# Optimization experiments

Hardware: AMD Instinct MI355X
Metric: run time of the kernel (lower is better)

## Reference

```python
import jax, jax.numpy as jnp
import numpy as np

B, OUT, IN = 2048, 4096, 4096
KEEPRATE = 0.5  # mid-training drop schedule state; first-call default masks nothing


def setup_inputs() -> dict:
    key = jax.random.key(0)
    k1, k2, k3, k4 = jax.random.split(key, 4)
    data = jax.random.normal(k1, (B, IN), dtype=jnp.float32)
    # weight parameter = fftn of a real N(0, 0.1) matrix, stored as complex
    w0 = jax.random.normal(k2, (OUT, IN), dtype=jnp.float32) * 0.1
    wc = jnp.fft.fftn(w0.astype(jnp.float32))
    w_real = jnp.real(wc).astype(jnp.float32)
    w_imag = jnp.imag(wc).astype(jnp.float32)
    bias = jax.random.normal(k3, (OUT,), dtype=jnp.float32) * 0.1
    # ZMAT: rank assignment, a permutation of 0..OUT*IN-1
    zmat = jax.random.permutation(k4, jnp.arange(OUT * IN, dtype=jnp.int64)).reshape(OUT, IN)
    return {"data": data, "w_real": w_real, "w_imag": w_imag, "bias": bias, "zmat": zmat}


def reference(data, w_real, w_imag, bias, zmat):
    O, I = w_real.shape
    numel = O * I
    threval = KEEPRATE * numel
    # IDROP: keep entries whose rank <= threshold (ZMAT > threval -> 0)
    idrop = (zmat.astype(jnp.float32) <= threval).astype(w_real.dtype)
    dropweight = (w_real + 1j * w_imag) * idrop  # masked FFT-domain weight
    # torch.fft.irfftn(dropweight, s=(O, I)): full ifft on dim 0, real irfft on dim 1
    # (numpy/jax irfft crops the last axis to I//2+1, same as torch)
    w_spatial = jnp.fft.irfftn(dropweight, s=(O, I), axes=(0, 1)).astype(data.dtype)
    return data @ w_spatial.T + bias
```

## Files before the change

kernel.cpp:

```cpp
#include <hip/hip_runtime.h>
#include <hip/hip_bf16.h>
#include <stdint.h>

#define OUT_N 4096
#define IN_N  4096
#define BATCH 2048
#define KHALF 2049

typedef __bf16 bf16x8 __attribute__((ext_vector_type(8)));
typedef float  f32x4  __attribute__((ext_vector_type(4)));

__device__ __forceinline__ unsigned short f2bf(float f) {
  unsigned int u = __builtin_bit_cast(unsigned int, f);
  u += 0x7FFFu + ((u >> 16) & 1u);
  return (unsigned short)(u >> 16);
}

__device__ __forceinline__ float2 cmul(float2 a, float2 b) {
  return make_float2(a.x * b.x - a.y * b.y, a.x * b.y + a.y * b.x);
}
__device__ __forceinline__ float2 cadd(float2 a, float2 b) { return make_float2(a.x + b.x, a.y + b.y); }
__device__ __forceinline__ float2 csub(float2 a, float2 b) { return make_float2(a.x - b.x, a.y - b.y); }
__device__ __forceinline__ float2 muli(float2 a) { return make_float2(-a.y, a.x); }

__device__ __forceinline__ void dft4i(float2& x0, float2& x1, float2& x2, float2& x3) {
  float2 t0 = cadd(x0, x2), t1 = csub(x0, x2);
  float2 t2 = cadd(x1, x3), t3 = csub(x1, x3);
  float2 it3 = muli(t3);
  x0 = cadd(t0, t2); x2 = csub(t0, t2);
  x1 = cadd(t1, it3); x3 = csub(t1, it3);
}

#define C8f  0.70710678118654752f
#define C16f 0.92387953251128676f
#define S16f 0.38268343236508977f

__device__ __forceinline__ void dft16i(float2 r[16]) {
  float2 t[16];
#pragma unroll
  for (int b = 0; b < 4; ++b) {
    float2 a0 = r[b], a1 = r[4 + b], a2 = r[8 + b], a3 = r[12 + b];
    dft4i(a0, a1, a2, a3);
    t[b * 4 + 0] = a0; t[b * 4 + 1] = a1; t[b * 4 + 2] = a2; t[b * 4 + 3] = a3;
  }
  const float2 W1 = make_float2(C16f, S16f);
  const float2 W2 = make_float2(C8f, C8f);
  const float2 W3 = make_float2(S16f, C16f);
  const float2 W6 = make_float2(-C8f, C8f);
  const float2 W9 = make_float2(-C16f, -S16f);
  t[5]  = cmul(t[5],  W1);  t[6]  = cmul(t[6],  W2);  t[7]  = cmul(t[7],  W3);
  t[9]  = cmul(t[9],  W2);  t[10] = muli(t[10]);      t[11] = cmul(t[11], W6);
  t[13] = cmul(t[13], W3);  t[14] = cmul(t[14], W6);  t[15] = cmul(t[15], W9);
#pragma unroll
  for (int q = 0; q < 4; ++q) {
    float2 a0 = t[q], a1 = t[4 + q], a2 = t[8 + q], a3 = t[12 + q];
    dft4i(a0, a1, a2, a3);
    r[q] = a0; r[q + 4] = a1; r[q + 8] = a2; r[q + 12] = a3;
  }
}

__device__ __forceinline__ void twiddle16(float2 r[16], float theta) {
  float sn, cs;
  __sincosf(theta, &sn, &cs);
  float2 w = make_float2(cs, sn);
  float2 wk = w;
  r[1] = cmul(r[1], wk);
#pragma unroll
  for (int k = 2; k < 16; ++k) {
    wk = cmul(wk, w);
    r[k] = cmul(r[k], wk);
  }
}

__device__ void fft4096_core(float2 r[16], float2* lds, int t) {
  dft16i(r);
  twiddle16(r, 1.53398078788564123e-3f * (float)t);
#pragma unroll
  for (int k1 = 0; k1 < 16; ++k1) lds[k1 * 257 + t] = r[k1];
  __syncthreads();
  const int k1 = t & 15, b = t >> 4;
  float2 s[16];
#pragma unroll
  for (int a = 0; a < 16; ++a) s[a] = lds[k1 * 257 + 16 * a + b];
  __syncthreads();
  dft16i(s);
  twiddle16(s, 2.45436926061702596e-2f * (float)b);
#pragma unroll
  for (int c = 0; c < 16; ++c) lds[k1 * 273 + c * 17 + b] = s[c];
  __syncthreads();
#pragma unroll
  for (int bb = 0; bb < 16; ++bb) r[bb] = lds[k1 * 273 + b * 17 + bb];
  dft16i(r);
}

__global__ void mask_transpose(const float* __restrict__ wr, const float* __restrict__ wi,
                               const int* __restrict__ zmat, float2* __restrict__ wt) {
  __shared__ float2 tile[32][33];
  const int k0 = blockIdx.x * 32;
  const int o0 = blockIdx.y * 32;
  const int tx = threadIdx.x;
  const int ty = threadIdx.y;
#pragma unroll
  for (int r = 0; r < 4; ++r) {
    int o = o0 + ty + r * 8;
    int k = k0 + tx;
    float2 v = make_float2(0.f, 0.f);
    if (k < KHALF) {
      size_t idx = (size_t)o * IN_N + k;
      if (zmat[idx] <= 8388608) v = make_float2(wr[idx], wi[idx]);
    }
    tile[ty + r * 8][tx] = v;
  }
  __syncthreads();
#pragma unroll
  for (int r = 0; r < 4; ++r) {
    int k = k0 + ty + r * 8;
    int o = o0 + tx;
    if (k < KHALF) wt[(size_t)k * OUT_N + o] = tile[tx][ty + r * 8];
  }
}

__global__ __launch_bounds__(256) void col_ifft(float2* __restrict__ wt) {
  __shared__ float2 lds[4368];
  const int t = threadIdx.x;
  float2* row = wt + (size_t)blockIdx.x * OUT_N;
  float2 r[16];
#pragma unroll
  for (int n1 = 0; n1 < 16; ++n1) r[n1] = row[n1 * 256 + t];
  fft4096_core(r, lds, t);
#pragma unroll
  for (int d = 0; d < 16; ++d) row[t + 256 * d] = r[d];
}

__global__ void transpose_ko(const float2* __restrict__ yt, float2* __restrict__ y) {
  __shared__ float2 tile[32][33];
  const int k0 = blockIdx.x * 32;
  const int o0 = blockIdx.y * 32;
  const int tx = threadIdx.x;
  const int ty = threadIdx.y;
#pragma unroll
  for (int r = 0; r < 4; ++r) {
    int k = k0 + ty + r * 8;
    int o = o0 + tx;
    if (k < KHALF) tile[ty + r * 8][tx] = yt[(size_t)k * OUT_N + o];
  }
  __syncthreads();
#pragma unroll
  for (int r = 0; r < 4; ++r) {
    int o = o0 + ty + r * 8;
    int k = k0 + tx;
    if (k < KHALF) y[(size_t)o * KHALF + k] = tile[tx][ty + r * 8];
  }
}

__global__ __launch_bounds__(256) void row_irfft2(const float2* __restrict__ y,
                                                  unsigned short* __restrict__ wbf) {
  __shared__ float2 lds[4368];
  const int t = threadIdx.x;
  const int oa = blockIdx.x * 2, ob = oa + 1;
  const float2* rowa = y + (size_t)oa * KHALF;
  const float2* rowb = y + (size_t)ob * KHALF;
  float2* lsa = lds;
  float2* lsb = lds + 2049;
#pragma unroll
  for (int j = 0; j < 9; ++j) {
    int k = t + j * 256;
    if (k < KHALF) { lsa[k] = rowa[k]; lsb[k] = rowb[k]; }
  }
  __syncthreads();
  float2 r[16];
#pragma unroll
  for (int n1 = 0; n1 < 16; ++n1) {
    int m = n1 * 256 + t;
    float2 za, zb;
    if (m == 0)        { za = make_float2(lsa[0].x, 0.f);    zb = make_float2(lsb[0].x, 0.f); }
    else if (m < 2048) { za = lsa[m];                        zb = lsb[m]; }
    else if (m == 2048){ za = make_float2(lsa[2048].x, 0.f); zb = make_float2(lsb[2048].x, 0.f); }
    else { float2 ua = lsa[4096 - m], ub = lsb[4096 - m];
           za = make_float2(ua.x, -ua.y); zb = make_float2(ub.x, -ub.y); }
    r[n1] = make_float2(za.x - zb.y, za.y + zb.x);
  }
  __syncthreads();
  fft4096_core(r, lds, t);
  const float sc = 1.0f / (4096.0f * 4096.0f);
  unsigned short* orow_a = wbf + (size_t)oa * IN_N;
  unsigned short* orow_b = wbf + (size_t)ob * IN_N;
#pragma unroll
  for (int d = 0; d < 16; ++d) {
    orow_a[t + 256 * d] = f2bf(r[d].x * sc);
    orow_b[t + 256 * d] = f2bf(r[d].y * sc);
  }
}

__global__ void cvt_bf16(const float* __restrict__ x, unsigned short* __restrict__ o, int n4) {
  int i = blockIdx.x * blockDim.x + threadIdx.x;
  if (i < n4) {
    float4 v = ((const float4*)x)[i];
    ushort4 r;
    r.x = f2bf(v.x); r.y = f2bf(v.y); r.z = f2bf(v.z); r.w = f2bf(v.w);
    ((ushort4*)o)[i] = r;
  }
}

__device__ __forceinline__ void gload_lds16(const void* gp, void* lp) {
  typedef const __attribute__((address_space(1))) void* gptr_t;
  typedef __attribute__((address_space(3))) void* lptr_t;
  __builtin_amdgcn_global_load_lds((gptr_t)(unsigned long long)gp,
                                   (lptr_t)(unsigned int)(unsigned long long)lp,
                                   16, 0, 0);
}

__global__ __launch_bounds__(512) void gemm_bt_bias(const unsigned short* __restrict__ A,
                                                    const unsigned short* __restrict__ B,
                                                    const float* __restrict__ bias,
                                                    float* __restrict__ C) {
  __shared__ __align__(16) unsigned short As[128 * 32];
  __shared__ __align__(16) unsigned short Bs[128 * 32];
  const int tid  = threadIdx.x;
  const int wave = tid >> 6;
  const int lane = tid & 63;
  const int gm0 = blockIdx.y * 128;
  const int gn0 = blockIdx.x * 128;

  f32x4 acc[4][2] = {};
  const int wm = wave >> 2, wn = wave & 3;
  const int lrow = lane >> 2;
  const int lcol = (lane & 3) * 8;
  const int rbase = wave * 16;

  for (int kt = 0; kt < IN_N; kt += 32) {
    gload_lds16(A + ((size_t)(gm0 + rbase + lrow) * IN_N + kt + lcol),
                As + (size_t)rbase * 32);
    gload_lds16(B + ((size_t)(gn0 + rbase + lrow) * IN_N + kt + lcol),
                Bs + (size_t)rbase * 32);
    __syncthreads();

    bf16x8 af[4], bfr[2];
#pragma unroll
    for (int i = 0; i < 4; ++i)
      af[i]  = *(const bf16x8*)&As[(wm * 64 + i * 16 + (lane & 15)) * 32 + (lane >> 4) * 8];
#pragma unroll
    for (int j = 0; j < 2; ++j)
      bfr[j] = *(const bf16x8*)&Bs[(wn * 32 + j * 16 + (lane & 15)) * 32 + (lane >> 4) * 8];
#pragma unroll
    for (int mi = 0; mi < 4; ++mi)
#pragma unroll
      for (int ni = 0; ni < 2; ++ni)
        acc[mi][ni] = __builtin_amdgcn_mfma_f32_16x16x32_bf16(af[mi], bfr[ni], acc[mi][ni], 0, 0, 0);
    __syncthreads();
  }

  const int col0 = gn0 + wn * 32 + (lane & 15);
  const int row0 = gm0 + wm * 64 + (lane >> 4) * 4;
#pragma unroll
  for (int mi = 0; mi < 4; ++mi) {
#pragma unroll
    for (int ni = 0; ni < 2; ++ni) {
      int col = col0 + ni * 16;
      float bv = bias[col];
#pragma unroll
      for (int r = 0; r < 4; ++r) {
        int row = row0 + mi * 16 + r;
        C[(size_t)row * OUT_N + col] = acc[mi][ni][r] + bv;
      }
    }
  }
}

extern "C" void kernel_launch(void* const* d_in, const int* in_sizes, int n_in,
                              void* d_out, int out_size, void* d_ws, size_t ws_size,
                              hipStream_t stream) {
  const float* data = (const float*)d_in[0];
  const float* wr   = (const float*)d_in[1];
  const float* wi   = (const float*)d_in[2];
  const float* bias = (const float*)d_in[3];
  const int*   zmat = (const int*)d_in[4];

  char* ws = (char*)d_ws;
  float2* wt = (float2*)ws;
  float2* y  = (float2*)(ws + 67141632ull);
  unsigned short* wbf = (unsigned short*)ws;
  unsigned short* dbf = (unsigned short*)(ws + 33554432ull);

  hipLaunchKernelGGL(mask_transpose, dim3(65, 128), dim3(32, 8), 0, stream, wr, wi, zmat, wt);
  hipLaunchKernelGGL(col_ifft,       dim3(2049),    dim3(256),   0, stream, wt);
  hipLaunchKernelGGL(transpose_ko,   dim3(65, 128), dim3(32, 8), 0, stream, wt, y);
  hipLaunchKernelGGL(row_irfft2,     dim3(2048),    dim3(256),   0, stream, y, wbf);
  hipLaunchKernelGGL(cvt_bf16,       dim3(8192),    dim3(256),   0, stream, data, dbf, (BATCH * IN_N) / 4);
  hipLaunchKernelGGL(gemm_bt_bias,   dim3(OUT_N / 128, BATCH / 128), dim3(512), 0, stream,
                     dbf, wbf, bias, (float*)d_out);
}
```

Measured before the change: 377.3 us.

## Enlarge GEMM per-wave tile with BK=64 swizzled LDS and widen mask_transpose tiles

The GEMM now runs 4 waves per block instead of 8. Each wave computes a 64x64 output tile instead of 64x32, and each step loads a K-slice of 64. LDS chunks are XOR-swizzled to avoid bank conflicts, which raises register reuse and halves the number of barriers per K. Separately, mask_transpose processes 64 columns per block with vectorized float2/int2 loads, plus a dedicated block for the Nyquist column. The larger accumulator set raises register pressure and may lower occupancy.

```diff
diff --git a/kernel.cpp b/kernel.cpp
--- a/kernel.cpp
+++ b/kernel.cpp
@@ -95,28 +95,38 @@
 
 __global__ void mask_transpose(const float* __restrict__ wr, const float* __restrict__ wi,
                                const int* __restrict__ zmat, float2* __restrict__ wt) {
-  __shared__ float2 tile[32][33];
-  const int k0 = blockIdx.x * 32;
-  const int o0 = blockIdx.y * 32;
+  __shared__ float2 tile[32][65];
   const int tx = threadIdx.x;
   const int ty = threadIdx.y;
+  const int o0 = blockIdx.y * 32;
+  if (blockIdx.x == 32) {
+    int t = ty * 32 + tx;
+    if (t < 32) {
+      int o = o0 + t;
+      size_t idx = (size_t)o * IN_N + 2048;
+      float2 v = make_float2(0.f, 0.f);
+      if (zmat[idx] <= 8388608) v = make_float2(wr[idx], wi[idx]);
+      wt[(size_t)2048 * OUT_N + o] = v;
+    }
+    return;
+  }
+  const int k0 = blockIdx.x * 64;
 #pragma unroll
   for (int r = 0; r < 4; ++r) {
     int o = o0 + ty + r * 8;
-    int k = k0 + tx;
-    float2 v = make_float2(0.f, 0.f);
-    if (k < KHALF) {
-      size_t idx = (size_t)o * IN_N + k;
-      if (zmat[idx] <= 8388608) v = make_float2(wr[idx], wi[idx]);
-    }
-    tile[ty + r * 8][tx] = v;
-  }
-  __syncthreads();
-#pragma unroll
-  for (int r = 0; r < 4; ++r) {
-    int k = k0 + ty + r * 8;
+    size_t base = (size_t)o * IN_N + k0 + tx * 2;
+    float2 vr = *(const float2*)&wr[base];
+    float2 vi = *(const float2*)&wi[base];
+    int2   z  = *(const int2*)&zmat[base];
+    tile[ty + r * 8][tx * 2]     = (z.x <= 8388608) ? make_float2(vr.x, vi.x) : make_float2(0.f, 0.f);
+    tile[ty + r * 8][tx * 2 + 1] = (z.y <= 8388608) ? make_float2(vr.y, vi.y) : make_float2(0.f, 0.f);
+  }
+  __syncthreads();
+#pragma unroll
+  for (int rr = 0; rr < 8; ++rr) {
+    int k = k0 + ty + rr * 8;
     int o = o0 + tx;
-    if (k < KHALF) wt[(size_t)k * OUT_N + o] = tile[tx][ty + r * 8];
+    wt[(size_t)k * OUT_N + o] = tile[tx][ty + rr * 8];
   }
 }
 
@@ -202,6 +212,8 @@
   }
 }
 
+#define BK 64
+
 __device__ __forceinline__ void gload_lds16(const void* gp, void* lp) {
   typedef const __attribute__((address_space(1))) void* gptr_t;
   typedef __attribute__((address_space(3))) void* lptr_t;
@@ -210,52 +222,62 @@
                                    16, 0, 0);
 }
 
-__global__ __launch_bounds__(512) void gemm_bt_bias(const unsigned short* __restrict__ A,
+__global__ __launch_bounds__(256) void gemm_bt_bias(const unsigned short* __restrict__ A,
                                                     const unsigned short* __restrict__ B,
                                                     const float* __restrict__ bias,
                                                     float* __restrict__ C) {
-  __shared__ __align__(16) unsigned short As[128 * 32];
-  __shared__ __align__(16) unsigned short Bs[128 * 32];
+  __shared__ __align__(16) unsigned short As[128 * BK];
+  __shared__ __align__(16) unsigned short Bs[128 * BK];
   const int tid  = threadIdx.x;
   const int wave = tid >> 6;
   const int lane = tid & 63;
   const int gm0 = blockIdx.y * 128;
   const int gn0 = blockIdx.x * 128;
 
-  f32x4 acc[4][2] = {};
-  const int wm = wave >> 2, wn = wave & 3;
-  const int lrow = lane >> 2;
-  const int lcol = (lane & 3) * 8;
-  const int rbase = wave * 16;
-
-  for (int kt = 0; kt < IN_N; kt += 32) {
-    gload_lds16(A + ((size_t)(gm0 + rbase + lrow) * IN_N + kt + lcol),
-                As + (size_t)rbase * 32);
-    gload_lds16(B + ((size_t)(gn0 + rbase + lrow) * IN_N + kt + lcol),
-                Bs + (size_t)rbase * 32);
+  f32x4 acc[4][4] = {};
+  const int wm = wave >> 1, wn = wave & 1;
+  const int srow   = lane >> 3;
+  const int schunk = (lane & 7) ^ srow;
+  const int l7 = lane & 7;
+  const int qbase = lane >> 4;
+  const int fra = wm * 64 + (lane & 15);
+  const int frb = wn * 64 + (lane & 15);
+
+  for (int kt = 0; kt < IN_N; kt += BK) {
+#pragma unroll
+    for (int j = 0; j < 4; ++j) {
+      const int r0 = wave * 32 + j * 8;
+      gload_lds16(A + ((size_t)(gm0 + r0 + srow) * IN_N + kt + schunk * 8),
+                  As + (size_t)r0 * BK);
+      gload_lds16(B + ((size_t)(gn0 + r0 + srow) * IN_N + kt + schunk * 8),
+                  Bs + (size_t)r0 * BK);
+    }
     __syncthreads();
 
-    bf16x8 af[4], bfr[2];
-#pragma unroll
-    for (int i = 0; i < 4; ++i)
-      af[i]  = *(const bf16x8*)&As[(wm * 64 + i * 16 + (lane & 15)) * 32 + (lane >> 4) * 8];
-#pragma unroll
-    for (int j = 0; j < 2; ++j)
-      bfr[j] = *(const bf16x8*)&Bs[(wn * 32 + j * 16 + (lane & 15)) * 32 + (lane >> 4) * 8];
-#pragma unroll
-    for (int mi = 0; mi < 4; ++mi)
-#pragma unroll
-      for (int ni = 0; ni < 2; ++ni)
-        acc[mi][ni] = __builtin_amdgcn_mfma_f32_16x16x32_bf16(af[mi], bfr[ni], acc[mi][ni], 0, 0, 0);
+#pragma unroll
+    for (int kk = 0; kk < 2; ++kk) {
+      bf16x8 af[4], bfr[4];
+      const int q = kk * 4 + qbase;
+#pragma unroll
+      for (int i = 0; i < 4; ++i) {
+        af[i]  = *(const bf16x8*)&As[(fra + i * 16) * BK + (q ^ l7) * 8];
+        bfr[i] = *(const bf16x8*)&Bs[(frb + i * 16) * BK + (q ^ l7) * 8];
+      }
+#pragma unroll
+      for (int mi = 0; mi < 4; ++mi)
+#pragma unroll
+        for (int ni = 0; ni < 4; ++ni)
+          acc[mi][ni] = __builtin_amdgcn_mfma_f32_16x16x32_bf16(af[mi], bfr[ni], acc[mi][ni], 0, 0, 0);
+    }
     __syncthreads();
   }
 
-  const int col0 = gn0 + wn * 32 + (lane & 15);
+  const int col0 = gn0 + wn * 64 + (lane & 15);
   const int row0 = gm0 + wm * 64 + (lane >> 4) * 4;
 #pragma unroll
   for (int mi = 0; mi < 4; ++mi) {
 #pragma unroll
-    for (int ni = 0; ni < 2; ++ni) {
+    for (int ni = 0; ni < 4; ++ni) {
       int col = col0 + ni * 16;
       float bv = bias[col];
 #pragma unroll
@@ -282,11 +304,11 @@
   unsigned short* wbf = (unsigned short*)ws;
   unsigned short* dbf = (unsigned short*)(ws + 33554432ull);
 
-  hipLaunchKernelGGL(mask_transpose, dim3(65, 128), dim3(32, 8), 0, stream, wr, wi, zmat, wt);
+  hipLaunchKernelGGL(mask_transpose, dim3(33, 128), dim3(32, 8), 0, stream, wr, wi, zmat, wt);
   hipLaunchKernelGGL(col_ifft,       dim3(2049),    dim3(256),   0, stream, wt);
   hipLaunchKernelGGL(transpose_ko,   dim3(65, 128), dim3(32, 8), 0, stream, wt, y);
   hipLaunchKernelGGL(row_irfft2,     dim3(2048),    dim3(256),   0, stream, y, wbf);
   hipLaunchKernelGGL(cvt_bf16,       dim3(8192),    dim3(256),   0, stream, data, dbf, (BATCH * IN_N) / 4);
-  hipLaunchKernelGGL(gemm_bt_bias,   dim3(OUT_N / 128, BATCH / 128), dim3(512), 0, stream,
+  hipLaunchKernelGGL(gemm_bt_bias,   dim3(OUT_N / 128, BATCH / 128), dim3(256), 0, stream,
                      dbf, wbf, bias, (float*)d_out);
 }
```

New measurement: 362.6 us. 1.04x faster.
